# Kernel tuning notes

Measured on AMD Instinct MI355X. Metric: run time of the kernel, lower is better.

Reference implementation:

```python
import math
import jax, jax.numpy as jnp
import numpy as np

B, T, D = 4, 2048, 1024
H = 16
DK = D // H


def setup_inputs() -> dict:
    key = jax.random.key(0)
    ks = jax.random.split(key, 9)
    s = 1.0 / math.sqrt(D)
    return {
        "x": jax.random.normal(ks[0], (B, T, D), dtype=jnp.float32),
        "Wq": jax.random.normal(ks[1], (D, D), dtype=jnp.float32) * s,
        "bq": jax.random.normal(ks[2], (D,), dtype=jnp.float32) * s,
        "Wk": jax.random.normal(ks[3], (D, D), dtype=jnp.float32) * s,
        "bk": jax.random.normal(ks[4], (D,), dtype=jnp.float32) * s,
        "Wv": jax.random.normal(ks[5], (D, D), dtype=jnp.float32) * s,
        "bv": jax.random.normal(ks[6], (D,), dtype=jnp.float32) * s,
        "Wo": jax.random.normal(ks[7], (D, D), dtype=jnp.float32) * s,
        "bo": jax.random.normal(ks[8], (D,), dtype=jnp.float32) * s,
    }


def reference(x, Wq, bq, Wk, bk, Wv, bv, Wo, bo):
    Bx, Tx, C = x.shape
    # projections -> [B, H, T, d_k]
    q = (x @ Wq + bq).reshape(Bx, Tx, H, DK).transpose(0, 2, 1, 3)
    k = (x @ Wk + bk).reshape(Bx, Tx, H, DK).transpose(0, 2, 1, 3)
    v = (x @ Wv + bv).reshape(Bx, Tx, H, DK).transpose(0, 2, 1, 3)
    # scores [B, H, T, T], scaled
    scores = jnp.einsum("bhqd,bhkd->bhqk", q, k) / math.sqrt(DK)
    causal = jnp.tril(jnp.ones((Tx, Tx), dtype=bool))
    scores = jnp.where(causal[None, None, :, :], scores, -jnp.inf)
    attn = jax.nn.softmax(scores, axis=-1)  # dropout p=0.0 (eval)
    out = jnp.einsum("bhqk,bhkd->bhqd", attn, v)
    out = out.transpose(0, 2, 1, 3).reshape(Bx, Tx, C)
    return out @ Wo + bo
```

## Files before the change

kernel.cpp:

```cpp
#include <hip/hip_runtime.h>
#include <stdint.h>
#include <math.h>

typedef __attribute__((ext_vector_type(8))) __bf16 bf16x8;
typedef __attribute__((ext_vector_type(4))) float f32x4;

__device__ __forceinline__ void load_lds16(const void* g, void* l) {
  __builtin_amdgcn_global_load_lds((__attribute__((address_space(1))) void*)(g),
                                   (__attribute__((address_space(3))) void*)(l),
                                   16, 0, 0);
}

__global__ __launch_bounds__(256)
void convert_x(const float* __restrict__ xf, __bf16* __restrict__ xb) {
  const size_t i = ((size_t)blockIdx.x * 256 + threadIdx.x) * 8;
  const float4 u0 = *(const float4*)(xf + i);
  const float4 u1 = *(const float4*)(xf + i + 4);
  bf16x8 v;
  v[0] = (__bf16)u0.x; v[1] = (__bf16)u0.y; v[2] = (__bf16)u0.z; v[3] = (__bf16)u0.w;
  v[4] = (__bf16)u1.x; v[5] = (__bf16)u1.y; v[6] = (__bf16)u1.z; v[7] = (__bf16)u1.w;
  *(bf16x8*)&xb[i] = v;
}

__global__ __launch_bounds__(256)
void prep_weights(const float* __restrict__ Wq, const float* __restrict__ Wk,
                  const float* __restrict__ Wv, const float* __restrict__ Wo,
                  const float* __restrict__ bq, const float* __restrict__ bk,
                  const float* __restrict__ bv, const float* __restrict__ bo,
                  __bf16* __restrict__ Bt1, __bf16* __restrict__ Bt2,
                  float* __restrict__ bqkv, float* __restrict__ bo_f) {
  const int m = blockIdx.z;
  const float* W = (m == 0) ? Wq : (m == 1) ? Wk : (m == 2) ? Wv : Wo;
  __bf16* Out = (m == 3) ? Bt2 : Bt1 + (size_t)m * 1024 * 1024;
  const int kt = blockIdx.x * 64, nt = blockIdx.y * 64;
  __shared__ __bf16 tile[64 * 68];
  const int t = threadIdx.x;
#pragma unroll
  for (int i = 0; i < 16; i++) {
    int e = i * 256 + t;
    int r = e >> 6, c = e & 63;
    tile[r * 68 + c] = (__bf16)W[(size_t)(kt + r) * 1024 + nt + c];
  }
  __syncthreads();
#pragma unroll
  for (int i = 0; i < 16; i++) {
    int e = i * 256 + t;
    int r = e >> 6, c = e & 63;
    Out[(size_t)(nt + r) * 1024 + kt + c] = tile[c * 68 + r];
  }
  if (blockIdx.x == 0 && blockIdx.y == 0) {
    if (m < 3) {
      const float* bsrc = (m == 0) ? bq : (m == 1) ? bk : bv;
      for (int i = t; i < 1024; i += 256) bqkv[m * 1024 + i] = bsrc[i];
    } else {
      for (int i = t; i < 1024; i += 256) bo_f[i] = bo[i];
    }
  }
}

__global__ __launch_bounds__(256)
void gemm_bt(const __bf16* __restrict__ A, const __bf16* __restrict__ Bt,
             const float* __restrict__ bias, void* __restrict__ Cv,
             int out_f32, int M, int N, int K) {
  __shared__ __align__(16) __bf16 As[128 * 32];
  __shared__ __align__(16) __bf16 Bs[128 * 32];
  const int t = threadIdx.x;
  const int lane = t & 63;
  const int wave = t >> 6;
  const int bm = blockIdx.x * 128;
  const int bn = blockIdx.y * 128;
  const int wm = (wave >> 1) * 64;
  const int wn = (wave & 1) * 64;
  const int fm = lane & 15, fk = (lane >> 4) * 8;
  f32x4 acc[4][4] = {};

  const int r0 = t >> 2, kc = (t & 3) * 8;
  const __bf16* Ag0 = A + (size_t)(bm + r0) * K + kc;
  const __bf16* Ag1 = A + (size_t)(bm + 64 + r0) * K + kc;
  const __bf16* Bg0 = Bt + (size_t)(bn + r0) * K + kc;
  const __bf16* Bg1 = Bt + (size_t)(bn + 64 + r0) * K + kc;

  for (int k0 = 0; k0 < K; k0 += 32) {
    load_lds16(Ag0 + k0, &As[t * 8]);
    load_lds16(Ag1 + k0, &As[2048 + t * 8]);
    load_lds16(Bg0 + k0, &Bs[t * 8]);
    load_lds16(Bg1 + k0, &Bs[2048 + t * 8]);
    asm volatile("s_waitcnt vmcnt(0)" ::: "memory");
    __syncthreads();
    bf16x8 af[4], bfr[4];
#pragma unroll
    for (int i = 0; i < 4; i++) {
      af[i] = *(const bf16x8*)&As[(wm + i * 16 + fm) * 32 + fk];
      bfr[i] = *(const bf16x8*)&Bs[(wn + i * 16 + fm) * 32 + fk];
    }
#pragma unroll
    for (int i = 0; i < 4; i++)
#pragma unroll
      for (int j = 0; j < 4; j++)
        acc[i][j] = __builtin_amdgcn_mfma_f32_16x16x32_bf16(af[i], bfr[j], acc[i][j], 0, 0, 0);
    __syncthreads();
  }

  const int cm = (lane >> 4) * 4, cn = lane & 15;
#pragma unroll
  for (int i = 0; i < 4; i++)
#pragma unroll
    for (int j = 0; j < 4; j++) {
      const int col = bn + wn + j * 16 + cn;
      const float bvv = bias[col];
#pragma unroll
      for (int r = 0; r < 4; r++) {
        const int row = bm + wm + i * 16 + cm + r;
        const float val = acc[i][j][r] + bvv;
        if (out_f32) ((float*)Cv)[(size_t)row * N + col] = val;
        else ((__bf16*)Cv)[(size_t)row * N + col] = (__bf16)val;
      }
    }
}

__global__ __launch_bounds__(256)
void transpose_v(const __bf16* __restrict__ QKV, __bf16* __restrict__ Vt) {
  const int tt = blockIdx.x;
  const int bh = blockIdx.y;
  const int b = bh >> 4, h = bh & 15;
  __shared__ __bf16 tile[64 * 68];
  const int t = threadIdx.x;
#pragma unroll
  for (int i = 0; i < 16; i++) {
    int e = i * 256 + t;
    int tok = e >> 6, dk = e & 63;
    tile[tok * 68 + dk] =
        QKV[((size_t)b * 2048 + tt * 64 + tok) * 3072 + 2048 + h * 64 + dk];
  }
  __syncthreads();
#pragma unroll
  for (int i = 0; i < 16; i++) {
    int e = i * 256 + t;
    int dk = e >> 6, tok = e & 63;
    Vt[((size_t)bh * 64 + dk) * 2048 + tt * 64 + tok] = tile[tok * 68 + dk];
  }
}

__global__ __launch_bounds__(256)
void flash_attn(const __bf16* __restrict__ QKV, const __bf16* __restrict__ Vt,
                __bf16* __restrict__ O) {
  const int pr = blockIdx.y;
  const int bh = blockIdx.x;
  const int b = bh >> 4, h = bh & 15;
  __shared__ __align__(16) __bf16 Ks[64 * 72];
  __shared__ __align__(16) __bf16 Vs[64 * 72];
  __shared__ __align__(16) __bf16 Ps[4 * 32 * 72];
  const int t = threadIdx.x, lane = t & 63, wave = t >> 6;
  const int fm = lane & 15, fq = lane >> 4;
  const int tok0 = t >> 3, ck = (t & 7) * 8;
  const size_t kbase = ((size_t)b * 2048) * 3072 + 1024 + h * 64;
  const size_t vbase = (size_t)bh * 64 * 2048;
  __bf16* Pw = &Ps[wave * 32 * 72];
  const float SC = 0.18033688011112042f;

  bf16x8 ones;
#pragma unroll
  for (int i = 0; i < 8; i++) ones[i] = (__bf16)1.0f;

  for (int half = 0; half < 2; half++) {
    const int qt = half ? pr : 15 - pr;
    const int nkt = 2 * qt + 2;
    const int qw = qt * 128 + wave * 32;
    const int qmax_w = qw + 31;

    bf16x8 qf[2][2];
#pragma unroll
    for (int mi = 0; mi < 2; mi++) {
      const size_t qrow =
          ((size_t)b * 2048 + qt * 128 + wave * 32 + mi * 16 + fm) * 3072 + h * 64;
      qf[mi][0] = *(const bf16x8*)&QKV[qrow + fq * 8];
      qf[mi][1] = *(const bf16x8*)&QKV[qrow + 32 + fq * 8];
    }

    f32x4 o_acc[2][4] = {};
    float m_i[2][4], l_i[2][4];
#pragma unroll
    for (int mi = 0; mi < 2; mi++)
#pragma unroll
      for (int r = 0; r < 4; r++) { m_i[mi][r] = -1e30f; l_i[mi][r] = 0.f; }

    bf16x8 pk0 = *(const bf16x8*)&QKV[kbase + (size_t)tok0 * 3072 + ck];
    bf16x8 pk1 = *(const bf16x8*)&QKV[kbase + (size_t)(32 + tok0) * 3072 + ck];
    bf16x8 pv0 = *(const bf16x8*)&Vt[vbase + (size_t)tok0 * 2048 + ck];
    bf16x8 pv1 = *(const bf16x8*)&Vt[vbase + (size_t)(32 + tok0) * 2048 + ck];

    for (int kt = 0; kt < nkt; kt++) {
      const int kb = kt * 64;
      __syncthreads();
      *(bf16x8*)&Ks[tok0 * 72 + ck] = pk0;
      *(bf16x8*)&Ks[(tok0 + 32) * 72 + ck] = pk1;
      *(bf16x8*)&Vs[tok0 * 72 + ck] = pv0;
      *(bf16x8*)&Vs[(tok0 + 32) * 72 + ck] = pv1;
      __syncthreads();

      if (kt + 1 < nkt) {
        const int kn = kb + 64;
        pk0 = *(const bf16x8*)&QKV[kbase + (size_t)(kn + tok0) * 3072 + ck];
        pk1 = *(const bf16x8*)&QKV[kbase + (size_t)(kn + 32 + tok0) * 3072 + ck];
        pv0 = *(const bf16x8*)&Vt[vbase + (size_t)tok0 * 2048 + kn + ck];
        pv1 = *(const bf16x8*)&Vt[vbase + (size_t)(32 + tok0) * 2048 + kn + ck];
      }

      if (kb > qmax_w) continue;

      f32x4 s[2][4];
#pragma unroll
      for (int nt = 0; nt < 4; nt++) {
        const bf16x8 kf0 = *(const bf16x8*)&Ks[(nt * 16 + fm) * 72 + fq * 8];
        const bf16x8 kf1 = *(const bf16x8*)&Ks[(nt * 16 + fm) * 72 + 32 + fq * 8];
#pragma unroll
        for (int mi = 0; mi < 2; mi++) {
          f32x4 z = {};
          z = __builtin_amdgcn_mfma_f32_16x16x32_bf16(qf[mi][0], kf0, z, 0, 0, 0);
          z = __builtin_amdgcn_mfma_f32_16x16x32_bf16(qf[mi][1], kf1, z, 0, 0, 0);
          s[mi][nt] = z;
        }
      }
      if (kb + 63 > qw) {
#pragma unroll
        for (int mi = 0; mi < 2; mi++) {
          const int qg = qw + mi * 16 + fq * 4;
#pragma unroll
          for (int nt = 0; nt < 4; nt++)
#pragma unroll
            for (int r = 0; r < 4; r++) {
              float v = s[mi][nt][r] * SC;
              if ((kb + nt * 16 + fm) > (qg + r)) v = -1e30f;
              s[mi][nt][r] = v;
            }
        }
      } else {
#pragma unroll
        for (int mi = 0; mi < 2; mi++)
#pragma unroll
          for (int nt = 0; nt < 4; nt++)
#pragma unroll
            for (int r = 0; r < 4; r++) s[mi][nt][r] *= SC;
      }

      float rmax[2][4];
#pragma unroll
      for (int mi = 0; mi < 2; mi++)
#pragma unroll
        for (int r = 0; r < 4; r++)
          rmax[mi][r] = fmaxf(fmaxf(s[mi][0][r], s[mi][1][r]),
                              fmaxf(s[mi][2][r], s[mi][3][r]));
#pragma unroll
      for (int off = 1; off < 16; off <<= 1)
#pragma unroll
        for (int mi = 0; mi < 2; mi++)
#pragma unroll
          for (int r = 0; r < 4; r++)
            rmax[mi][r] = fmaxf(rmax[mi][r], __shfl_xor(rmax[mi][r], off, 64));

      float grow = -1e30f;
#pragma unroll
      for (int mi = 0; mi < 2; mi++)
#pragma unroll
        for (int r = 0; r < 4; r++) grow = fmaxf(grow, rmax[mi][r] - m_i[mi][r]);
      if (!__all(grow <= 8.0f)) {
#pragma unroll
        for (int mi = 0; mi < 2; mi++) {
          float a[4];
#pragma unroll
          for (int r = 0; r < 4; r++) {
            const float mn = fmaxf(m_i[mi][r], rmax[mi][r]);
            a[r] = exp2f(m_i[mi][r] - mn);
            m_i[mi][r] = mn;
            l_i[mi][r] *= a[r];
          }
#pragma unroll
          for (int dt = 0; dt < 4; dt++)
#pragma unroll
            for (int r = 0; r < 4; r++) o_acc[mi][dt][r] *= a[r];
        }
      }

#pragma unroll
      for (int mi = 0; mi < 2; mi++)
#pragma unroll
        for (int nt = 0; nt < 4; nt++)
#pragma unroll
          for (int r = 0; r < 4; r++)
            Pw[(mi * 16 + fq * 4 + r) * 72 + nt * 16 + fm] =
                (__bf16)exp2f(s[mi][nt][r] - m_i[mi][r]);

      bf16x8 pf[2][2];
#pragma unroll
      for (int mi = 0; mi < 2; mi++) {
        pf[mi][0] = *(const bf16x8*)&Pw[(mi * 16 + fm) * 72 + fq * 8];
        pf[mi][1] = *(const bf16x8*)&Pw[(mi * 16 + fm) * 72 + 32 + fq * 8];
      }

#pragma unroll
      for (int mi = 0; mi < 2; mi++) {
        f32x4 rs = {};
        rs = __builtin_amdgcn_mfma_f32_16x16x32_bf16(pf[mi][0], ones, rs, 0, 0, 0);
        rs = __builtin_amdgcn_mfma_f32_16x16x32_bf16(pf[mi][1], ones, rs, 0, 0, 0);
#pragma unroll
        for (int r = 0; r < 4; r++) l_i[mi][r] += rs[r];
      }

#pragma unroll
      for (int dt = 0; dt < 4; dt++) {
        const bf16x8 vf0 = *(const bf16x8*)&Vs[(dt * 16 + fm) * 72 + fq * 8];
        const bf16x8 vf1 = *(const bf16x8*)&Vs[(dt * 16 + fm) * 72 + 32 + fq * 8];
#pragma unroll
        for (int mi = 0; mi < 2; mi++) {
          f32x4 o = o_acc[mi][dt];
          o = __builtin_amdgcn_mfma_f32_16x16x32_bf16(pf[mi][0], vf0, o, 0, 0, 0);
          o = __builtin_amdgcn_mfma_f32_16x16x32_bf16(pf[mi][1], vf1, o, 0, 0, 0);
          o_acc[mi][dt] = o;
        }
      }
    }

#pragma unroll
    for (int mi = 0; mi < 2; mi++)
#pragma unroll
      for (int r = 0; r < 4; r++) l_i[mi][r] = 1.f / l_i[mi][r];
#pragma unroll
    for (int mi = 0; mi < 2; mi++) {
      const size_t orow = (size_t)b * 2048 + qt * 128 + wave * 32 + mi * 16 + fq * 4;
#pragma unroll
      for (int dt = 0; dt < 4; dt++)
#pragma unroll
        for (int r = 0; r < 4; r++)
          O[(orow + r) * 1024 + h * 64 + dt * 16 + fm] =
              (__bf16)(o_acc[mi][dt][r] * l_i[mi][r]);
    }
  }
}

extern "C" void kernel_launch(void* const* d_in, const int* in_sizes, int n_in,
                              void* d_out, int out_size, void* d_ws, size_t ws_size,
                              hipStream_t stream) {
  const float* x = (const float*)d_in[0];
  const float* Wq = (const float*)d_in[1];
  const float* bq = (const float*)d_in[2];
  const float* Wk = (const float*)d_in[3];
  const float* bk = (const float*)d_in[4];
  const float* Wv = (const float*)d_in[5];
  const float* bv = (const float*)d_in[6];
  const float* Wo = (const float*)d_in[7];
  const float* bo = (const float*)d_in[8];

  char* ws = (char*)d_ws;
  __bf16* Bt1 = (__bf16*)(ws);
  __bf16* Bt2 = (__bf16*)(ws + 6291456);
  float* bqkv = (float*)(ws + 8388608);
  float* bo_f = (float*)(ws + 8400896);
  __bf16* QKV = (__bf16*)(ws + 8405504);
  __bf16* Vt = (__bf16*)(ws + 58737152);
  __bf16* Xb = (__bf16*)(ws + 75514368);
  __bf16* Ow = Xb;

  hipLaunchKernelGGL(convert_x, dim3(4096), dim3(256), 0, stream, x, Xb);
  hipLaunchKernelGGL(prep_weights, dim3(16, 16, 4), dim3(256), 0, stream,
                     Wq, Wk, Wv, Wo, bq, bk, bv, bo, Bt1, Bt2, bqkv, bo_f);
  hipLaunchKernelGGL(gemm_bt, dim3(64, 24), dim3(256), 0, stream,
                     Xb, Bt1, bqkv, (void*)QKV, 0, 8192, 3072, 1024);
  hipLaunchKernelGGL(transpose_v, dim3(32, 64), dim3(256), 0, stream, QKV, Vt);
  hipLaunchKernelGGL(flash_attn, dim3(64, 8), dim3(256), 0, stream, QKV, Vt, Ow);
  hipLaunchKernelGGL(gemm_bt, dim3(64, 8), dim3(256), 0, stream,
                     Ow, Bt2, bo_f, d_out, 1, 8192, 1024, 1024);
}
```

Before: 366.2 us.

## Restructure flash attention with async double-buffered LDS and in-register P

Loads K/V tiles into double-buffered, XOR-swizzled LDS via global_load_lds, removing the register staging and one barrier per tile. Computes S transposed so each lane owns a query row, which allows row max and sum with only two shuffles. P is repacked through lane shuffles instead of an LDS round trip, and the ones-MFMA row sum is dropped. Each block now handles one q-tile instead of a balanced pair, in a 16-wide interleaved grid ordering, and setprio is raised around the MFMA sections. The risk is more shuffle work per tile and less even work per block.

```diff
diff --git a/kernel.cpp b/kernel.cpp
--- a/kernel.cpp
+++ b/kernel.cpp
@@ -3,12 +3,19 @@
 #include <math.h>
 
 typedef __attribute__((ext_vector_type(8))) __bf16 bf16x8;
+typedef __attribute__((ext_vector_type(4))) __bf16 bf16x4;
 typedef __attribute__((ext_vector_type(4))) float f32x4;
 
 __device__ __forceinline__ void load_lds16(const void* g, void* l) {
   __builtin_amdgcn_global_load_lds((__attribute__((address_space(1))) void*)(g),
                                    (__attribute__((address_space(3))) void*)(l),
                                    16, 0, 0);
+}
+
+__device__ __forceinline__ uint32_t pack_bf2(float a, float b) {
+  union { __bf16 h; uint16_t u; } x, y;
+  x.h = (__bf16)a; y.h = (__bf16)b;
+  return (uint32_t)x.u | ((uint32_t)y.u << 16);
 }
 
 __global__ __launch_bounds__(256)
@@ -144,95 +151,101 @@
 __global__ __launch_bounds__(256)
 void flash_attn(const __bf16* __restrict__ QKV, const __bf16* __restrict__ Vt,
                 __bf16* __restrict__ O) {
-  const int pr = blockIdx.y;
+  const int y = blockIdx.y;
+  const int g = y >> 2, iy = y & 3;
+  const int qt = (g == 0) ? (15 - 2 * iy)
+               : (g == 1) ? (2 * iy)
+               : (g == 2) ? (14 - 2 * iy)
+                          : (2 * iy + 1);
   const int bh = blockIdx.x;
   const int b = bh >> 4, h = bh & 15;
-  __shared__ __align__(16) __bf16 Ks[64 * 72];
-  __shared__ __align__(16) __bf16 Vs[64 * 72];
-  __shared__ __align__(16) __bf16 Ps[4 * 32 * 72];
+  __shared__ __align__(16) __bf16 Ks[2][64 * 64];
+  __shared__ __align__(16) __bf16 Vs[2][64 * 64];
   const int t = threadIdx.x, lane = t & 63, wave = t >> 6;
   const int fm = lane & 15, fq = lane >> 4;
-  const int tok0 = t >> 3, ck = (t & 7) * 8;
+  const int tok0 = t >> 3;
+  const int csw = ((t & 7) ^ (tok0 & 7)) << 3;
+  const int swb = (fm & 7) << 4;
+  const int rb0 = (((fq << 4)) ^ swb) >> 1;
+  const int rb1 = ((64 + (fq << 4)) ^ swb) >> 1;
+
   const size_t kbase = ((size_t)b * 2048) * 3072 + 1024 + h * 64;
   const size_t vbase = (size_t)bh * 64 * 2048;
-  __bf16* Pw = &Ps[wave * 32 * 72];
+  const int nkt = 2 * qt + 2;
+  const int qw = qt * 128 + wave * 32;
+  const int qmax_w = qw + 31;
   const float SC = 0.18033688011112042f;
 
-  bf16x8 ones;
-#pragma unroll
-  for (int i = 0; i < 8; i++) ones[i] = (__bf16)1.0f;
-
-  for (int half = 0; half < 2; half++) {
-    const int qt = half ? pr : 15 - pr;
-    const int nkt = 2 * qt + 2;
-    const int qw = qt * 128 + wave * 32;
-    const int qmax_w = qw + 31;
-
-    bf16x8 qf[2][2];
-#pragma unroll
-    for (int mi = 0; mi < 2; mi++) {
-      const size_t qrow =
-          ((size_t)b * 2048 + qt * 128 + wave * 32 + mi * 16 + fm) * 3072 + h * 64;
-      qf[mi][0] = *(const bf16x8*)&QKV[qrow + fq * 8];
-      qf[mi][1] = *(const bf16x8*)&QKV[qrow + 32 + fq * 8];
-    }
-
-    f32x4 o_acc[2][4] = {};
-    float m_i[2][4], l_i[2][4];
-#pragma unroll
-    for (int mi = 0; mi < 2; mi++)
-#pragma unroll
-      for (int r = 0; r < 4; r++) { m_i[mi][r] = -1e30f; l_i[mi][r] = 0.f; }
-
-    bf16x8 pk0 = *(const bf16x8*)&QKV[kbase + (size_t)tok0 * 3072 + ck];
-    bf16x8 pk1 = *(const bf16x8*)&QKV[kbase + (size_t)(32 + tok0) * 3072 + ck];
-    bf16x8 pv0 = *(const bf16x8*)&Vt[vbase + (size_t)tok0 * 2048 + ck];
-    bf16x8 pv1 = *(const bf16x8*)&Vt[vbase + (size_t)(32 + tok0) * 2048 + ck];
-
-    for (int kt = 0; kt < nkt; kt++) {
-      const int kb = kt * 64;
-      __syncthreads();
-      *(bf16x8*)&Ks[tok0 * 72 + ck] = pk0;
-      *(bf16x8*)&Ks[(tok0 + 32) * 72 + ck] = pk1;
-      *(bf16x8*)&Vs[tok0 * 72 + ck] = pv0;
-      *(bf16x8*)&Vs[(tok0 + 32) * 72 + ck] = pv1;
-      __syncthreads();
-
-      if (kt + 1 < nkt) {
-        const int kn = kb + 64;
-        pk0 = *(const bf16x8*)&QKV[kbase + (size_t)(kn + tok0) * 3072 + ck];
-        pk1 = *(const bf16x8*)&QKV[kbase + (size_t)(kn + 32 + tok0) * 3072 + ck];
-        pv0 = *(const bf16x8*)&Vt[vbase + (size_t)tok0 * 2048 + kn + ck];
-        pv1 = *(const bf16x8*)&Vt[vbase + (size_t)(32 + tok0) * 2048 + kn + ck];
-      }
-
-      if (kb > qmax_w) continue;
+  bf16x8 qf[2][2];
+#pragma unroll
+  for (int mi = 0; mi < 2; mi++) {
+    const size_t qrow = ((size_t)b * 2048 + qw + mi * 16 + fm) * 3072 + h * 64;
+    qf[mi][0] = *(const bf16x8*)&QKV[qrow + fq * 8];
+    qf[mi][1] = *(const bf16x8*)&QKV[qrow + 32 + fq * 8];
+  }
+
+  f32x4 o_acc[2][4] = {};
+  float m_i[2] = {-1e30f, -1e30f}, l_i[2] = {0.f, 0.f};
+
+  const int srcA = ((lane & 16) << 1) | fm;
+  const int srcB = srcA + 16;
+  const bool sel_hi = (lane & 32) != 0;
+
+#define STAGE(KT, BUF)                                                          \
+  {                                                                             \
+    const int kb2 = (KT) * 64;                                                  \
+    load_lds16(&QKV[kbase + (size_t)(kb2 + tok0) * 3072 + csw],                 \
+               &Ks[BUF][t * 8]);                                                \
+    load_lds16(&QKV[kbase + (size_t)(kb2 + 32 + tok0) * 3072 + csw],            \
+               &Ks[BUF][2048 + t * 8]);                                         \
+    load_lds16(&Vt[vbase + (size_t)tok0 * 2048 + kb2 + csw],                    \
+               &Vs[BUF][t * 8]);                                                \
+    load_lds16(&Vt[vbase + (size_t)(tok0 + 32) * 2048 + kb2 + csw],             \
+               &Vs[BUF][2048 + t * 8]);                                         \
+  }
+
+  STAGE(0, 0);
+  __syncthreads();
+  int cur = 0;
+
+  for (int kt = 0; kt < nkt; kt++) {
+    const int kb = kt * 64;
+    if (kt + 1 < nkt) STAGE(kt + 1, cur ^ 1);
+
+    if (kb <= qmax_w) {
+      const __bf16* Kc = Ks[cur];
+      const __bf16* Vc = Vs[cur];
 
       f32x4 s[2][4];
+      __builtin_amdgcn_s_setprio(1);
 #pragma unroll
       for (int nt = 0; nt < 4; nt++) {
-        const bf16x8 kf0 = *(const bf16x8*)&Ks[(nt * 16 + fm) * 72 + fq * 8];
-        const bf16x8 kf1 = *(const bf16x8*)&Ks[(nt * 16 + fm) * 72 + 32 + fq * 8];
+        const bf16x8 kf0 = *(const bf16x8*)&Kc[(nt * 16 + fm) * 64 + rb0];
+        const bf16x8 kf1 = *(const bf16x8*)&Kc[(nt * 16 + fm) * 64 + rb1];
 #pragma unroll
         for (int mi = 0; mi < 2; mi++) {
           f32x4 z = {};
-          z = __builtin_amdgcn_mfma_f32_16x16x32_bf16(qf[mi][0], kf0, z, 0, 0, 0);
-          z = __builtin_amdgcn_mfma_f32_16x16x32_bf16(qf[mi][1], kf1, z, 0, 0, 0);
+          z = __builtin_amdgcn_mfma_f32_16x16x32_bf16(kf0, qf[mi][0], z, 0, 0, 0);
+          z = __builtin_amdgcn_mfma_f32_16x16x32_bf16(kf1, qf[mi][1], z, 0, 0, 0);
           s[mi][nt] = z;
         }
       }
+      __builtin_amdgcn_s_setprio(0);
+
       if (kb + 63 > qw) {
 #pragma unroll
         for (int mi = 0; mi < 2; mi++) {
-          const int qg = qw + mi * 16 + fq * 4;
-#pragma unroll
-          for (int nt = 0; nt < 4; nt++)
+          const int qq = qw + mi * 16 + fm;
+#pragma unroll
+          for (int nt = 0; nt < 4; nt++) {
+            const int kk = kb + nt * 16 + fq * 4;
 #pragma unroll
             for (int r = 0; r < 4; r++) {
               float v = s[mi][nt][r] * SC;
-              if ((kb + nt * 16 + fm) > (qg + r)) v = -1e30f;
+              if (kk + r > qq) v = -1e30f;
               s[mi][nt][r] = v;
             }
+          }
         }
       } else {
 #pragma unroll
@@ -243,98 +256,113 @@
             for (int r = 0; r < 4; r++) s[mi][nt][r] *= SC;
       }
 
-      float rmax[2][4];
+      float rmax[2];
+#pragma unroll
+      for (int mi = 0; mi < 2; mi++) {
+        float a = fmaxf(fmaxf(s[mi][0][0], s[mi][0][1]),
+                        fmaxf(s[mi][0][2], s[mi][0][3]));
+#pragma unroll
+        for (int nt = 1; nt < 4; nt++)
+          a = fmaxf(a, fmaxf(fmaxf(s[mi][nt][0], s[mi][nt][1]),
+                             fmaxf(s[mi][nt][2], s[mi][nt][3])));
+        a = fmaxf(a, __shfl_xor(a, 16, 64));
+        a = fmaxf(a, __shfl_xor(a, 32, 64));
+        rmax[mi] = a;
+      }
+
+      const float grow = fmaxf(rmax[0] - m_i[0], rmax[1] - m_i[1]);
+      if (!__all(grow <= 8.0f)) {
+#pragma unroll
+        for (int mi = 0; mi < 2; mi++) {
+          const float mn = fmaxf(m_i[mi], rmax[mi]);
+          const float a = exp2f(m_i[mi] - mn);
+          m_i[mi] = mn;
+          l_i[mi] *= a;
+#pragma unroll
+          for (int dt = 0; dt < 4; dt++)
+#pragma unroll
+            for (int r = 0; r < 4; r++) o_acc[mi][dt][r] *= a;
+        }
+      }
+
+#pragma unroll
+      for (int mi = 0; mi < 2; mi++) {
+        float sum = 0.f;
+#pragma unroll
+        for (int nt = 0; nt < 4; nt++)
+#pragma unroll
+          for (int r = 0; r < 4; r++) {
+            const float p = exp2f(s[mi][nt][r] - m_i[mi]);
+            s[mi][nt][r] = p;
+            sum += p;
+          }
+        sum += __shfl_xor(sum, 16, 64);
+        sum += __shfl_xor(sum, 32, 64);
+        l_i[mi] += sum;
+      }
+
+      uint32_t u[2][4][2];
 #pragma unroll
       for (int mi = 0; mi < 2; mi++)
 #pragma unroll
-        for (int r = 0; r < 4; r++)
-          rmax[mi][r] = fmaxf(fmaxf(s[mi][0][r], s[mi][1][r]),
-                              fmaxf(s[mi][2][r], s[mi][3][r]));
-#pragma unroll
-      for (int off = 1; off < 16; off <<= 1)
-#pragma unroll
-        for (int mi = 0; mi < 2; mi++)
-#pragma unroll
-          for (int r = 0; r < 4; r++)
-            rmax[mi][r] = fmaxf(rmax[mi][r], __shfl_xor(rmax[mi][r], off, 64));
-
-      float grow = -1e30f;
+        for (int nt = 0; nt < 4; nt++) {
+          u[mi][nt][0] = pack_bf2(s[mi][nt][0], s[mi][nt][1]);
+          u[mi][nt][1] = pack_bf2(s[mi][nt][2], s[mi][nt][3]);
+        }
+
+      union U8 { bf16x8 v; uint32_t d[4]; };
+      U8 pb[2][2];
 #pragma unroll
       for (int mi = 0; mi < 2; mi++)
 #pragma unroll
-        for (int r = 0; r < 4; r++) grow = fmaxf(grow, rmax[mi][r] - m_i[mi][r]);
-      if (!__all(grow <= 8.0f)) {
-#pragma unroll
-        for (int mi = 0; mi < 2; mi++) {
-          float a[4];
-#pragma unroll
-          for (int r = 0; r < 4; r++) {
-            const float mn = fmaxf(m_i[mi][r], rmax[mi][r]);
-            a[r] = exp2f(m_i[mi][r] - mn);
-            m_i[mi][r] = mn;
-            l_i[mi][r] *= a[r];
-          }
-#pragma unroll
-          for (int dt = 0; dt < 4; dt++)
-#pragma unroll
-            for (int r = 0; r < 4; r++) o_acc[mi][dt][r] *= a[r];
-        }
-      }
-
-#pragma unroll
-      for (int mi = 0; mi < 2; mi++)
-#pragma unroll
-        for (int nt = 0; nt < 4; nt++)
-#pragma unroll
-          for (int r = 0; r < 4; r++)
-            Pw[(mi * 16 + fq * 4 + r) * 72 + nt * 16 + fm] =
-                (__bf16)exp2f(s[mi][nt][r] - m_i[mi][r]);
-
-      bf16x8 pf[2][2];
-#pragma unroll
-      for (int mi = 0; mi < 2; mi++) {
-        pf[mi][0] = *(const bf16x8*)&Pw[(mi * 16 + fm) * 72 + fq * 8];
-        pf[mi][1] = *(const bf16x8*)&Pw[(mi * 16 + fm) * 72 + 32 + fq * 8];
-      }
-
-#pragma unroll
-      for (int mi = 0; mi < 2; mi++) {
-        f32x4 rs = {};
-        rs = __builtin_amdgcn_mfma_f32_16x16x32_bf16(pf[mi][0], ones, rs, 0, 0, 0);
-        rs = __builtin_amdgcn_mfma_f32_16x16x32_bf16(pf[mi][1], ones, rs, 0, 0, 0);
-#pragma unroll
-        for (int r = 0; r < 4; r++) l_i[mi][r] += rs[r];
-      }
-
+        for (int c = 0; c < 2; c++) {
+          const uint32_t a0 = __shfl((int)u[mi][2 * c][0], srcA, 64);
+          const uint32_t b0 = __shfl((int)u[mi][2 * c + 1][0], srcA, 64);
+          const uint32_t a1 = __shfl((int)u[mi][2 * c][1], srcA, 64);
+          const uint32_t b1 = __shfl((int)u[mi][2 * c + 1][1], srcA, 64);
+          const uint32_t a2 = __shfl((int)u[mi][2 * c][0], srcB, 64);
+          const uint32_t b2 = __shfl((int)u[mi][2 * c + 1][0], srcB, 64);
+          const uint32_t a3 = __shfl((int)u[mi][2 * c][1], srcB, 64);
+          const uint32_t b3 = __shfl((int)u[mi][2 * c + 1][1], srcB, 64);
+          pb[mi][c].d[0] = sel_hi ? b0 : a0;
+          pb[mi][c].d[1] = sel_hi ? b1 : a1;
+          pb[mi][c].d[2] = sel_hi ? b2 : a2;
+          pb[mi][c].d[3] = sel_hi ? b3 : a3;
+        }
+
+      __builtin_amdgcn_s_setprio(1);
 #pragma unroll
       for (int dt = 0; dt < 4; dt++) {
-        const bf16x8 vf0 = *(const bf16x8*)&Vs[(dt * 16 + fm) * 72 + fq * 8];
-        const bf16x8 vf1 = *(const bf16x8*)&Vs[(dt * 16 + fm) * 72 + 32 + fq * 8];
+        const bf16x8 vf0 = *(const bf16x8*)&Vc[(dt * 16 + fm) * 64 + rb0];
+        const bf16x8 vf1 = *(const bf16x8*)&Vc[(dt * 16 + fm) * 64 + rb1];
 #pragma unroll
         for (int mi = 0; mi < 2; mi++) {
           f32x4 o = o_acc[mi][dt];
-          o = __builtin_amdgcn_mfma_f32_16x16x32_bf16(pf[mi][0], vf0, o, 0, 0, 0);
-          o = __builtin_amdgcn_mfma_f32_16x16x32_bf16(pf[mi][1], vf1, o, 0, 0, 0);
+          o = __builtin_amdgcn_mfma_f32_16x16x32_bf16(vf0, pb[mi][0].v, o, 0, 0, 0);
+          o = __builtin_amdgcn_mfma_f32_16x16x32_bf16(vf1, pb[mi][1].v, o, 0, 0, 0);
           o_acc[mi][dt] = o;
         }
       }
+      __builtin_amdgcn_s_setprio(0);
     }
 
-#pragma unroll
-    for (int mi = 0; mi < 2; mi++)
-#pragma unroll
-      for (int r = 0; r < 4; r++) l_i[mi][r] = 1.f / l_i[mi][r];
-#pragma unroll
-    for (int mi = 0; mi < 2; mi++) {
-      const size_t orow = (size_t)b * 2048 + qt * 128 + wave * 32 + mi * 16 + fq * 4;
-#pragma unroll
-      for (int dt = 0; dt < 4; dt++)
-#pragma unroll
-        for (int r = 0; r < 4; r++)
-          O[(orow + r) * 1024 + h * 64 + dt * 16 + fm] =
-              (__bf16)(o_acc[mi][dt][r] * l_i[mi][r]);
+    __syncthreads();
+    cur ^= 1;
+  }
+
+#pragma unroll
+  for (int mi = 0; mi < 2; mi++) {
+    const float linv = 1.f / l_i[mi];
+    const size_t orow = (size_t)b * 2048 + qw + mi * 16 + fm;
+#pragma unroll
+    for (int dt = 0; dt < 4; dt++) {
+      bf16x4 w;
+#pragma unroll
+      for (int r = 0; r < 4; r++) w[r] = (__bf16)(o_acc[mi][dt][r] * linv);
+      *(bf16x4*)&O[orow * 1024 + h * 64 + dt * 16 + fq * 4] = w;
     }
   }
+#undef STAGE
 }
 
 extern "C" void kernel_launch(void* const* d_in, const int* in_sizes, int n_in,
@@ -366,7 +394,7 @@
   hipLaunchKernelGGL(gemm_bt, dim3(64, 24), dim3(256), 0, stream,
                      Xb, Bt1, bqkv, (void*)QKV, 0, 8192, 3072, 1024);
   hipLaunchKernelGGL(transpose_v, dim3(32, 64), dim3(256), 0, stream, QKV, Vt);
-  hipLaunchKernelGGL(flash_attn, dim3(64, 8), dim3(256), 0, stream, QKV, Vt, Ow);
+  hipLaunchKernelGGL(flash_attn, dim3(64, 16), dim3(256), 0, stream, QKV, Vt, Ow);
   hipLaunchKernelGGL(gemm_bt, dim3(64, 8), dim3(256), 0, stream,
                      Ow, Bt2, bo_f, d_out, 1, 8192, 1024, 1024);
 }
```

Result: faster. 326.8 us (-10.8%).
